# Kernel optimization log

Hardware: AMD Instinct MI355X
Metric: run time of the kernel (lower is better)

Reference implementation:

```python
import jax, jax.numpy as jnp
import numpy as np


def _mlp(x, Ws):
    # torch Linear(bias=False): y = x @ W.T, then leaky_relu (slope 0.01)
    for W in Ws:
        x = jax.nn.leaky_relu(x @ W.T)
    return x


def setup_inputs() -> dict:
    key = jax.random.key(0)
    ks = jax.random.split(key, 17)
    B, Cm, Hm = 128, 512, 28
    D = 2048  # NET_OUT_DIM['resnet50']
    shapes = {
        'x_mid': (B, Cm, Hm, Hm),
        'x_deep': (B, D, 7, 7),
        'w_shallow': (D, Cm),
        'ow1': (1024, D), 'ow2': (512, 1024), 'ow3': (64, 512),
        'sw1': (1024, D), 'sw2': (512, 1024), 'sw3': (64, 512),
        'tw1': (64, 128), 'tw2': (64, 64),
        'cw1': (64, 128), 'cw2': (64, 64),
        'qw1': (64, 64), 'qw2': (64, 64),
        'center': (64,), 'proto': (4, 64),
    }
    out = {}
    for k, (name, shp) in zip(ks, shapes.items()):
        scale = 1.0 if name in ('x_mid', 'x_deep', 'center', 'proto') else 0.02
        out[name] = jax.random.normal(k, shp, dtype=jnp.float32) * scale
    return out


def reference(x_mid, x_deep, w_shallow, ow1, ow2, ow3, sw1, sw2, sw3,
              tw1, tw2, cw1, cw2, qw1, qw2, center, proto):
    # shallow_conv: 1x1 conv Cm -> D
    shallow_map = jnp.einsum('bchw,oc->bohw', x_mid, w_shallow)
    # adaptive avgpool (1,1) + flatten == mean over HW
    origin = _mlp(x_deep.mean(axis=(2, 3)), [ow1, ow2, ow3])        # [B,64]
    shallow = _mlp(shallow_map.mean(axis=(2, 3)), [sw1, sw2, sw3])  # [B,64]
    texture = _mlp(jnp.concatenate([shallow, shallow - center[None]], axis=1),
                   [tw1, tw2])                                      # [B,64]
    # squared distances to each domain prototype -> [B, domain_cnt]
    sim = jnp.sum((texture[:, None, :] - proto[None, :, :]) ** 2, axis=-1)
    category = jnp.argmax(sim, axis=1)  # argmax(softmax(x)) == argmax(x)
    logp = jax.nn.log_softmax(sim, axis=1)
    ce = -jnp.mean(jnp.take_along_axis(logp, category[:, None], axis=1))
    # vectorized gather of per-sample prototype (replaces python loop)
    class_feat = jnp.concatenate([origin, origin - proto[category]], axis=1)
    class_feat = _mlp(class_feat, [cw1, cw2])
    class_svdd = jnp.sum((class_feat - center[None]) ** 2, axis=1)
    origin_svdd = jnp.sum((_mlp(origin, [qw1, qw2]) - center[None]) ** 2, axis=1)
    align = jnp.abs(origin_svdd - class_svdd)
    return jnp.stack([ce, origin_svdd.mean(), class_svdd.mean(),
                      align.mean()]).reshape(4, 1)
```

## Files before the change

kernel.cpp:

```cpp
#include <hip/hip_runtime.h>
#include <hip/hip_bf16.h>
#include <math.h>

typedef __attribute__((ext_vector_type(8))) short bf16x8;
typedef __attribute__((ext_vector_type(4))) float f32x4;
typedef __attribute__((ext_vector_type(4))) unsigned short u16x4;

__device__ __forceinline__ float leaky(float x) { return x > 0.0f ? x : 0.01f * x; }

__device__ __forceinline__ unsigned short f2b(float f) {
    unsigned u = __builtin_bit_cast(unsigned, f);
    u += 0x7fffu + ((u >> 16) & 1u);
    return (unsigned short)(u >> 16);
}

__device__ __forceinline__ bf16x8 cvt8(float4 u0, float4 u1) {
    bf16x8 r;
    r[0] = (short)f2b(u0.x); r[1] = (short)f2b(u0.y);
    r[2] = (short)f2b(u0.z); r[3] = (short)f2b(u0.w);
    r[4] = (short)f2b(u1.x); r[5] = (short)f2b(u1.y);
    r[6] = (short)f2b(u1.z); r[7] = (short)f2b(u1.w);
    return r;
}

__global__ __launch_bounds__(256) void prep_kernel(
    const float* __restrict__ xm, const float* __restrict__ xd,
    const float* __restrict__ sw1, const float* __restrict__ wsh,
    unsigned short* __restrict__ Ws1,
    unsigned short* __restrict__ xm_b, unsigned short* __restrict__ xd_b,
    float4* __restrict__ zbase)
{
    const int blk = blockIdx.x;
    const int tid = threadIdx.x;

    if (blk < 256) {
        const int l = tid & 63, lr = l & 15, lc = l >> 4, w = tid >> 6;
        const int m0 = (blk >> 4) * 64 + w * 16;
        const int n0 = (blk & 15) * 32;
        const float* ap = sw1 + (size_t)(m0 + lr) * 2048 + lc * 8;
        f32x4 acc0 = {0.f,0.f,0.f,0.f}, acc1 = {0.f,0.f,0.f,0.f};
        for (int kt = 0; kt < 2048; kt += 32) {
            bf16x8 a = cvt8(*(const float4*)(ap + kt), *(const float4*)(ap + kt + 4));
            bf16x8 b0, b1;
            #pragma unroll
            for (int j = 0; j < 8; ++j) {
                int kk = kt + lc * 8 + j;
                b0[j] = (short)f2b(wsh[(size_t)kk * 512 + n0 + lr]);
                b1[j] = (short)f2b(wsh[(size_t)kk * 512 + n0 + 16 + lr]);
            }
            acc0 = __builtin_amdgcn_mfma_f32_16x16x32_bf16(a, b0, acc0, 0, 0, 0);
            acc1 = __builtin_amdgcn_mfma_f32_16x16x32_bf16(a, b1, acc1, 0, 0, 0);
        }
        #pragma unroll
        for (int r = 0; r < 4; ++r) {
            int m = m0 + lc * 4 + r;
            Ws1[(size_t)m * 512 + n0 + lr]      = f2b(acc0[r]);
            Ws1[(size_t)m * 512 + n0 + 16 + lr] = f2b(acc1[r]);
        }
        return;
    }
    if (blk < 16640) {
        int b2 = blk - 256;
        int lane = tid & 63, wid = tid >> 6;
        int row  = b2 * 4 + wid;
        const float4* r = (const float4*)(xm + (size_t)row * 784);
        float s = 0.0f;
        for (int i = lane; i < 196; i += 64) {
            float4 v = r[i];
            s += v.x + v.y + v.z + v.w;
        }
        #pragma unroll
        for (int off = 32; off; off >>= 1) s += __shfl_xor(s, off);
        if (lane == 0) xm_b[row] = f2b(s * (1.0f / 784.0f));
        return;
    }
    if (blk < 33024) {
        int b3 = blk - 16640;
        int sub = tid & 15, rr = tid >> 4;
        int row = b3 * 16 + rr;
        const float* base = xd + (size_t)row * 49;
        float s = base[sub] + base[sub + 16] + base[sub + 32];
        if (sub == 0) s += base[48];
        #pragma unroll
        for (int off = 8; off; off >>= 1) s += __shfl_xor(s, off);
        if (sub == 0) xd_b[row] = f2b(s * (1.0f / 49.0f));
        return;
    }
    {
        int idx = (blk - 33024) * 256 + tid;
        zbase[idx] = make_float4(0.f, 0.f, 0.f, 0.f);
    }
}

__device__ __forceinline__ void gemm_phase(
    const void* __restrict__ A, int af, int aact,
    const void* __restrict__ B, int bfB,
    float* __restrict__ C,
    int N, int K, int Kc, int k0, int n0,
    unsigned short (*Bs)[72], int tid)
{
    const int l  = tid & 63;
    const int lr = l & 15;
    const int lc = l >> 4;
    const int m0 = (tid >> 6) * 16;
    const int srow = tid >> 4;
    const int scol = (tid & 15) * 4;

    f32x4 acc0 = {0.f,0.f,0.f,0.f}, acc1 = {0.f,0.f,0.f,0.f};

    for (int kt = 0; kt < Kc; kt += 64) {
        if (!bfB) {
            float4 v = *(const float4*)((const float*)B + (size_t)(n0 + srow) * K + k0 + kt + scol);
            __syncthreads();
            Bs[srow][scol + 0] = f2b(v.x);
            Bs[srow][scol + 1] = f2b(v.y);
            Bs[srow][scol + 2] = f2b(v.z);
            Bs[srow][scol + 3] = f2b(v.w);
        } else {
            u16x4 v = *(const u16x4*)((const unsigned short*)B + (size_t)(n0 + srow) * K + k0 + kt + scol);
            __syncthreads();
            Bs[srow][scol + 0] = v.x;
            Bs[srow][scol + 1] = v.y;
            Bs[srow][scol + 2] = v.z;
            Bs[srow][scol + 3] = v.w;
        }
        __syncthreads();

        #pragma unroll
        for (int kc = 0; kc < 2; ++kc) {
            size_t aoff = (size_t)(m0 + lr) * K + k0 + kt + kc * 32 + lc * 8;
            bf16x8 a;
            if (!af) {
                a = *(const bf16x8*)((const unsigned short*)A + aoff);
            } else {
                const float* p = (const float*)A + aoff;
                float4 u0 = *(const float4*)p;
                float4 u1 = *(const float4*)(p + 4);
                if (aact) {
                    u0.x = leaky(u0.x); u0.y = leaky(u0.y);
                    u0.z = leaky(u0.z); u0.w = leaky(u0.w);
                    u1.x = leaky(u1.x); u1.y = leaky(u1.y);
                    u1.z = leaky(u1.z); u1.w = leaky(u1.w);
                }
                a = cvt8(u0, u1);
            }
            bf16x8 b0 = *(const bf16x8*)&Bs[lr][kc * 32 + lc * 8];
            bf16x8 b1 = *(const bf16x8*)&Bs[16 + lr][kc * 32 + lc * 8];
            acc0 = __builtin_amdgcn_mfma_f32_16x16x32_bf16(a, b0, acc0, 0, 0, 0);
            acc1 = __builtin_amdgcn_mfma_f32_16x16x32_bf16(a, b1, acc1, 0, 0, 0);
        }
    }

    #pragma unroll
    for (int r = 0; r < 4; ++r) {
        int m = m0 + lc * 4 + r;
        atomicAdd(&C[(size_t)m * N + n0 + lr],      acc0[r]);
        atomicAdd(&C[(size_t)m * N + n0 + 16 + lr], acc1[r]);
    }
}

__global__ __launch_bounds__(512) void l1_kernel(
    const unsigned short* __restrict__ xd_b, const unsigned short* __restrict__ xm_b,
    const float* __restrict__ ow1, const unsigned short* __restrict__ Ws1,
    float* __restrict__ C2o, float* __restrict__ C2s)
{
    __shared__ unsigned short Bs[32][72];
    const int bid = blockIdx.x, tid = threadIdx.x;
    if (bid < 256) {
        int nt = bid >> 3, s = bid & 7;
        gemm_phase(xd_b, 0, 0, ow1, 0, C2o, 1024, 2048, 256, s * 256, nt * 32, Bs, tid);
    } else {
        int idx = bid - 256, nt = idx >> 2, s = idx & 3;
        gemm_phase(xm_b, 0, 0, Ws1, 1, C2s, 1024, 512, 128, s * 128, nt * 32, Bs, tid);
    }
}

__global__ __launch_bounds__(512) void l2_kernel(
    const float* __restrict__ C2o, const float* __restrict__ C2s,
    const float* __restrict__ ow2, const float* __restrict__ sw2,
    float* __restrict__ C3o, float* __restrict__ C3s)
{
    __shared__ unsigned short Bs[32][72];
    const int bid = blockIdx.x, tid = threadIdx.x;
    const int z = bid >> 7, idx = bid & 127;
    const int nt = idx >> 3, s = idx & 7;
    gemm_phase(z ? (const void*)C2s : (const void*)C2o, 1, 1,
               z ? (const void*)sw2 : (const void*)ow2, 0,
               z ? C3s : C3o, 512, 1024, 128, s * 128, nt * 32, Bs, tid);
}

__global__ __launch_bounds__(256) void tail_kernel(
    const float* __restrict__ C3o, const float* __restrict__ C3s,
    const float* __restrict__ ow3, const float* __restrict__ sw3,
    const float* __restrict__ tw1, const float* __restrict__ tw2,
    const float* __restrict__ cw1, const float* __restrict__ cw2,
    const float* __restrict__ qw1, const float* __restrict__ qw2,
    const float* __restrict__ center, const float* __restrict__ proto,
    int* __restrict__ cnt, float* __restrict__ ce_t, float* __restrict__ osv,
    float* __restrict__ csv, float* __restrict__ alv,
    float* __restrict__ out)
{
    const int b = blockIdx.x;
    const int tid = threadIdx.x;
    __shared__ float o2r[512], s2r[512];
    __shared__ float red[2][64][4];
    __shared__ float o3s[64], s3s[64], t1s[64], c1s[64], q1s[64];
    __shared__ float tmp[4][4];
    __shared__ int flag;

    for (int e = tid; e < 512; e += 256) {
        o2r[e] = leaky(C3o[b * 512 + e]);
        s2r[e] = leaky(C3s[b * 512 + e]);
    }
    __syncthreads();
    {
        int o = (tid >> 2) & 63, q = tid & 3, p = tid >> 8;
        (void)p;
        const float* wro = ow3 + (size_t)o * 512 + q * 128;
        const float* wrs = sw3 + (size_t)o * 512 + q * 128;
        const float* xo = o2r + q * 128;
        const float* xs = s2r + q * 128;
        float ao = 0.f, as_ = 0.f;
        for (int j = 0; j < 128; ++j) {
            ao  += wro[j] * xo[j];
            as_ += wrs[j] * xs[j];
        }
        red[0][o][q] = ao;
        red[1][o][q] = as_;
    }
    __syncthreads();
    if (tid < 128) {
        int p = tid >> 6, o = tid & 63;
        float v = leaky(red[p][o][0] + red[p][o][1] + red[p][o][2] + red[p][o][3]);
        if (p) s3s[o] = v; else o3s[o] = v;
    }
    __syncthreads();

    float ce_val = 0.f;
    int o = tid;
    if (tid < 64) {
        float acc = 0.f;
        for (int j = 0; j < 64; ++j) acc += tw1[o * 128 + j] * s3s[j];
        for (int j = 0; j < 64; ++j) acc += tw1[o * 128 + 64 + j] * (s3s[j] - center[j]);
        t1s[o] = leaky(acc);
    }
    __syncthreads();
    if (tid < 64) {
        float acc = 0.f;
        for (int j = 0; j < 64; ++j) acc += tw2[o * 64 + j] * t1s[j];
        float tex = leaky(acc);
        float sim[4];
        #pragma unroll
        for (int k = 0; k < 4; ++k) {
            float d = tex - proto[k * 64 + o];
            float v = d * d;
            #pragma unroll
            for (int off = 32; off; off >>= 1) v += __shfl_xor(v, off);
            sim[k] = v;
        }
        int cat = 0; float best = sim[0];
        #pragma unroll
        for (int k = 1; k < 4; ++k) if (sim[k] > best) { best = sim[k]; cat = k; }
        float sume = 0.f;
        #pragma unroll
        for (int k = 0; k < 4; ++k) sume += expf(sim[k] - best);
        ce_val = logf(sume);
        float acc2 = 0.f;
        for (int j = 0; j < 64; ++j) acc2 += cw1[o * 128 + j] * o3s[j];
        for (int j = 0; j < 64; ++j) acc2 += cw1[o * 128 + 64 + j] * (o3s[j] - proto[cat * 64 + j]);
        c1s[o] = leaky(acc2);
        acc2 = 0.f;
        for (int j = 0; j < 64; ++j) acc2 += qw1[o * 64 + j] * o3s[j];
        q1s[o] = leaky(acc2);
    }
    __syncthreads();
    if (tid < 64) {
        float acc = 0.f;
        for (int j = 0; j < 64; ++j) acc += cw2[o * 64 + j] * c1s[j];
        float cf = leaky(acc);
        float dc = cf - center[o];
        float cs = dc * dc;
        #pragma unroll
        for (int off = 32; off; off >>= 1) cs += __shfl_xor(cs, off);
        acc = 0.f;
        for (int j = 0; j < 64; ++j) acc += qw2[o * 64 + j] * q1s[j];
        float qf = leaky(acc);
        float dq = qf - center[o];
        float os = dq * dq;
        #pragma unroll
        for (int off = 32; off; off >>= 1) os += __shfl_xor(os, off);
        if (o == 0) {
            __hip_atomic_store(&ce_t[b], ce_val, __ATOMIC_RELAXED, __HIP_MEMORY_SCOPE_AGENT);
            __hip_atomic_store(&osv[b],  os,     __ATOMIC_RELAXED, __HIP_MEMORY_SCOPE_AGENT);
            __hip_atomic_store(&csv[b],  cs,     __ATOMIC_RELAXED, __HIP_MEMORY_SCOPE_AGENT);
            __hip_atomic_store(&alv[b],  fabsf(os - cs), __ATOMIC_RELAXED, __HIP_MEMORY_SCOPE_AGENT);
        }
    }
    __syncthreads();
    if (tid == 0) {
        asm volatile("s_waitcnt vmcnt(0)" ::: "memory");
        int old = __hip_atomic_fetch_add(cnt, 1, __ATOMIC_ACQ_REL, __HIP_MEMORY_SCOPE_AGENT);
        flag = (old == 127);
    }
    __syncthreads();
    if (flag) {
        float v0 = 0.f, v1 = 0.f, v2 = 0.f, v3 = 0.f;
        if (tid < 128) {
            v0 = __hip_atomic_load(&ce_t[tid], __ATOMIC_RELAXED, __HIP_MEMORY_SCOPE_AGENT);
            v1 = __hip_atomic_load(&osv[tid],  __ATOMIC_RELAXED, __HIP_MEMORY_SCOPE_AGENT);
            v2 = __hip_atomic_load(&csv[tid],  __ATOMIC_RELAXED, __HIP_MEMORY_SCOPE_AGENT);
            v3 = __hip_atomic_load(&alv[tid],  __ATOMIC_RELAXED, __HIP_MEMORY_SCOPE_AGENT);
        }
        float v[4] = { v0, v1, v2, v3 };
        int lane = tid & 63, wv = tid >> 6;
        #pragma unroll
        for (int i = 0; i < 4; ++i) {
            float x = v[i];
            #pragma unroll
            for (int off = 32; off; off >>= 1) x += __shfl_xor(x, off);
            if (lane == 0) tmp[i][wv] = x;
        }
        __syncthreads();
        if (tid < 4) {
            float s = 0.f;
            #pragma unroll
            for (int j = 0; j < 4; ++j) s += tmp[tid][j];
            out[tid] = s * (1.0f / 128.0f);
        }
    }
}

extern "C" void kernel_launch(void* const* d_in, const int* in_sizes, int n_in,
                              void* d_out, int out_size, void* d_ws, size_t ws_size,
                              hipStream_t stream)
{
    const float* x_mid     = (const float*)d_in[0];
    const float* x_deep    = (const float*)d_in[1];
    const float* w_shallow = (const float*)d_in[2];
    const float* ow1 = (const float*)d_in[3];
    const float* ow2 = (const float*)d_in[4];
    const float* ow3 = (const float*)d_in[5];
    const float* sw1 = (const float*)d_in[6];
    const float* sw2 = (const float*)d_in[7];
    const float* sw3 = (const float*)d_in[8];
    const float* tw1 = (const float*)d_in[9];
    const float* tw2 = (const float*)d_in[10];
    const float* cw1 = (const float*)d_in[11];
    const float* cw2 = (const float*)d_in[12];
    const float* qw1 = (const float*)d_in[13];
    const float* qw2 = (const float*)d_in[14];
    const float* center = (const float*)d_in[15];
    const float* proto  = (const float*)d_in[16];
    float* out = (float*)d_out;

    float* wf = (float*)d_ws;
    float* C2o = wf;
    float* C2s = wf + 131072;
    float* C3o = wf + 262144;
    float* C3s = wf + 327680;
    int*   cnt = (int*)(wf + 393216);
    float* ce_t = wf + 393472;
    float* osv  = ce_t + 128;
    float* csv  = ce_t + 256;
    float* alv  = ce_t + 384;
    unsigned short* Ws1  = (unsigned short*)(wf + 394240);
    unsigned short* xm_b = Ws1 + 524288;
    unsigned short* xd_b = xm_b + 65536;

    prep_kernel<<<33409, 256, 0, stream>>>(x_mid, x_deep, sw1, w_shallow,
                                           Ws1, xm_b, xd_b, (float4*)wf);

    l1_kernel<<<384, 512, 0, stream>>>(xd_b, xm_b, ow1, Ws1, C2o, C2s);

    l2_kernel<<<256, 512, 0, stream>>>(C2o, C2s, ow2, sw2, C3o, C3s);

    tail_kernel<<<128, 256, 0, stream>>>(C3o, C3s, ow3, sw3, tw1, tw2, cw1, cw2,
                                         qw1, qw2, center, proto,
                                         cnt, ce_t, osv, csv, alv, out);
}
```

Before: 99.94 us.

## Fuse GEMM layers and tail into one kernel with flag-gated stages

Merges the two GEMM layer kernels and the tail kernel into a single 768-block launch. Later stages spin on global counter and flag words before reading earlier results, which removes two kernel launch boundaries. The prep kernel's weight-fold GEMM is also retiled into 32 larger blocks, each computing a 128x128 tile so A and B fragments are reused more. The spin-wait relies on all producer blocks being resident or scheduled first, which carries a deadlock or stall risk, and the retiled fold runs on far fewer blocks.

New measurement: 169.3 us. 1.69x slower.

```diff
diff --git a/kernel.cpp b/kernel.cpp
--- a/kernel.cpp
+++ b/kernel.cpp
@@ -33,34 +33,55 @@
     const int blk = blockIdx.x;
     const int tid = threadIdx.x;
 
-    if (blk < 256) {
+    if (blk < 32) {
+        const int mb = blk >> 2, nb = blk & 3;
         const int l = tid & 63, lr = l & 15, lc = l >> 4, w = tid >> 6;
-        const int m0 = (blk >> 4) * 64 + w * 16;
-        const int n0 = (blk & 15) * 32;
-        const float* ap = sw1 + (size_t)(m0 + lr) * 2048 + lc * 8;
-        f32x4 acc0 = {0.f,0.f,0.f,0.f}, acc1 = {0.f,0.f,0.f,0.f};
+        const int m0 = mb * 128 + w * 32;
+        const int n0 = nb * 128;
+        const float* ap0 = sw1 + (size_t)(m0 + lr) * 2048 + lc * 8;
+        const float* ap1 = ap0 + (size_t)16 * 2048;
+        f32x4 acc[2][4][2];
+        #pragma unroll
+        for (int a = 0; a < 2; ++a)
+            #pragma unroll
+            for (int b = 0; b < 4; ++b)
+                #pragma unroll
+                for (int c = 0; c < 2; ++c) acc[a][b][c] = (f32x4){0.f,0.f,0.f,0.f};
+
         for (int kt = 0; kt < 2048; kt += 32) {
-            bf16x8 a = cvt8(*(const float4*)(ap + kt), *(const float4*)(ap + kt + 4));
-            bf16x8 b0, b1;
-            #pragma unroll
-            for (int j = 0; j < 8; ++j) {
-                int kk = kt + lc * 8 + j;
-                b0[j] = (short)f2b(wsh[(size_t)kk * 512 + n0 + lr]);
-                b1[j] = (short)f2b(wsh[(size_t)kk * 512 + n0 + 16 + lr]);
+            bf16x8 a0 = cvt8(*(const float4*)(ap0 + kt), *(const float4*)(ap0 + kt + 4));
+            bf16x8 a1 = cvt8(*(const float4*)(ap1 + kt), *(const float4*)(ap1 + kt + 4));
+            #pragma unroll
+            for (int nf = 0; nf < 4; ++nf) {
+                bf16x8 b0, b1;
+                #pragma unroll
+                for (int j = 0; j < 8; ++j) {
+                    const float* bp = wsh + (size_t)(kt + lc * 8 + j) * 512 + n0 + nf * 32 + lr;
+                    b0[j] = (short)f2b(bp[0]);
+                    b1[j] = (short)f2b(bp[16]);
+                }
+                acc[0][nf][0] = __builtin_amdgcn_mfma_f32_16x16x32_bf16(a0, b0, acc[0][nf][0], 0, 0, 0);
+                acc[0][nf][1] = __builtin_amdgcn_mfma_f32_16x16x32_bf16(a0, b1, acc[0][nf][1], 0, 0, 0);
+                acc[1][nf][0] = __builtin_amdgcn_mfma_f32_16x16x32_bf16(a1, b0, acc[1][nf][0], 0, 0, 0);
+                acc[1][nf][1] = __builtin_amdgcn_mfma_f32_16x16x32_bf16(a1, b1, acc[1][nf][1], 0, 0, 0);
             }
-            acc0 = __builtin_amdgcn_mfma_f32_16x16x32_bf16(a, b0, acc0, 0, 0, 0);
-            acc1 = __builtin_amdgcn_mfma_f32_16x16x32_bf16(a, b1, acc1, 0, 0, 0);
-        }
-        #pragma unroll
-        for (int r = 0; r < 4; ++r) {
-            int m = m0 + lc * 4 + r;
-            Ws1[(size_t)m * 512 + n0 + lr]      = f2b(acc0[r]);
-            Ws1[(size_t)m * 512 + n0 + 16 + lr] = f2b(acc1[r]);
-        }
-        return;
-    }
-    if (blk < 16640) {
-        int b2 = blk - 256;
+        }
+        #pragma unroll
+        for (int mf = 0; mf < 2; ++mf)
+            #pragma unroll
+            for (int nf = 0; nf < 4; ++nf)
+                #pragma unroll
+                for (int p = 0; p < 2; ++p)
+                    #pragma unroll
+                    for (int r = 0; r < 4; ++r) {
+                        int m = m0 + mf * 16 + lc * 4 + r;
+                        int n = n0 + nf * 32 + p * 16 + lr;
+                        Ws1[(size_t)m * 512 + n] = f2b(acc[mf][nf][p][r]);
+                    }
+        return;
+    }
+    if (blk < 16416) {
+        int b2 = blk - 32;
         int lane = tid & 63, wid = tid >> 6;
         int row  = b2 * 4 + wid;
         const float4* r = (const float4*)(xm + (size_t)row * 784);
@@ -74,8 +95,8 @@
         if (lane == 0) xm_b[row] = f2b(s * (1.0f / 784.0f));
         return;
     }
-    if (blk < 33024) {
-        int b3 = blk - 16640;
+    if (blk < 32800) {
+        int b3 = blk - 16416;
         int sub = tid & 15, rr = tid >> 4;
         int row = b3 * 16 + rr;
         const float* base = xd + (size_t)row * 49;
@@ -87,8 +108,27 @@
         return;
     }
     {
-        int idx = (blk - 33024) * 256 + tid;
+        int idx = (blk - 32800) * 256 + tid;
         zbase[idx] = make_float4(0.f, 0.f, 0.f, 0.f);
+    }
+}
+
+__device__ __forceinline__ void gate(const int* flag) {
+    if (threadIdx.x == 0) {
+        while (__hip_atomic_load(flag, __ATOMIC_RELAXED, __HIP_MEMORY_SCOPE_AGENT) == 0)
+            __builtin_amdgcn_s_sleep(32);
+    }
+    __syncthreads();
+    __builtin_amdgcn_fence(__ATOMIC_ACQUIRE, "agent");
+}
+
+__device__ __forceinline__ void done(int* cnt, int target, int* flag) {
+    __syncthreads();
+    if (threadIdx.x == 0) {
+        asm volatile("s_waitcnt vmcnt(0)" ::: "memory");
+        int old = __hip_atomic_fetch_add(cnt, 1, __ATOMIC_RELAXED, __HIP_MEMORY_SCOPE_AGENT);
+        if (old == target - 1)
+            __hip_atomic_store(flag, 1, __ATOMIC_RELAXED, __HIP_MEMORY_SCOPE_AGENT);
     }
 }
 
@@ -159,74 +199,81 @@
     }
 }
 
-__global__ __launch_bounds__(512) void l1_kernel(
-    const unsigned short* __restrict__ xd_b, const unsigned short* __restrict__ xm_b,
-    const float* __restrict__ ow1, const unsigned short* __restrict__ Ws1,
-    float* __restrict__ C2o, float* __restrict__ C2s)
-{
-    __shared__ unsigned short Bs[32][72];
-    const int bid = blockIdx.x, tid = threadIdx.x;
-    if (bid < 256) {
-        int nt = bid >> 3, s = bid & 7;
-        gemm_phase(xd_b, 0, 0, ow1, 0, C2o, 1024, 2048, 256, s * 256, nt * 32, Bs, tid);
-    } else {
-        int idx = bid - 256, nt = idx >> 2, s = idx & 3;
-        gemm_phase(xm_b, 0, 0, Ws1, 1, C2s, 1024, 512, 128, s * 128, nt * 32, Bs, tid);
-    }
-}
-
-__global__ __launch_bounds__(512) void l2_kernel(
-    const float* __restrict__ C2o, const float* __restrict__ C2s,
-    const float* __restrict__ ow2, const float* __restrict__ sw2,
-    float* __restrict__ C3o, float* __restrict__ C3s)
-{
-    __shared__ unsigned short Bs[32][72];
-    const int bid = blockIdx.x, tid = threadIdx.x;
-    const int z = bid >> 7, idx = bid & 127;
-    const int nt = idx >> 3, s = idx & 7;
-    gemm_phase(z ? (const void*)C2s : (const void*)C2o, 1, 1,
-               z ? (const void*)sw2 : (const void*)ow2, 0,
-               z ? C3s : C3o, 512, 1024, 128, s * 128, nt * 32, Bs, tid);
-}
-
-__global__ __launch_bounds__(256) void tail_kernel(
-    const float* __restrict__ C3o, const float* __restrict__ C3s,
-    const float* __restrict__ ow3, const float* __restrict__ sw3,
+__global__ __launch_bounds__(512, 4) void fused_kernel(
+    float* __restrict__ wf,
+    const unsigned short* __restrict__ xm_b, const unsigned short* __restrict__ xd_b,
+    const unsigned short* __restrict__ Ws1,
+    const float* __restrict__ ow1, const float* __restrict__ ow2, const float* __restrict__ ow3,
+    const float* __restrict__ sw2, const float* __restrict__ sw3,
     const float* __restrict__ tw1, const float* __restrict__ tw2,
     const float* __restrict__ cw1, const float* __restrict__ cw2,
     const float* __restrict__ qw1, const float* __restrict__ qw2,
     const float* __restrict__ center, const float* __restrict__ proto,
-    int* __restrict__ cnt, float* __restrict__ ce_t, float* __restrict__ osv,
-    float* __restrict__ csv, float* __restrict__ alv,
     float* __restrict__ out)
 {
-    const int b = blockIdx.x;
-    const int tid = threadIdx.x;
+    __shared__ unsigned short Bs[32][72];
     __shared__ float o2r[512], s2r[512];
     __shared__ float red[2][64][4];
     __shared__ float o3s[64], s3s[64], t1s[64], c1s[64], q1s[64];
-    __shared__ float tmp[4][4];
-    __shared__ int flag;
-
-    for (int e = tid; e < 512; e += 256) {
+    __shared__ float tmp[4][8];
+    __shared__ int flag_sh;
+
+    float* C2o = wf;
+    float* C2s = wf + 131072;
+    float* C3o = wf + 262144;
+    float* C3s = wf + 327680;
+    int*   cntL1  = (int*)(wf + 393216);
+    int*   flagL1 = (int*)(wf + 393216 + 32);
+    int*   cntL2  = (int*)(wf + 393216 + 64);
+    int*   flagL2 = (int*)(wf + 393216 + 96);
+    int*   cntT   = (int*)(wf + 393216 + 128);
+    float* ce_t = wf + 393472;
+    float* osv  = ce_t + 128;
+    float* csv  = ce_t + 256;
+    float* alv  = ce_t + 384;
+
+    const int bid = blockIdx.x;
+    const int tid = threadIdx.x;
+
+    if (bid < 256) {
+        int nt = bid >> 3, s = bid & 7;
+        gemm_phase(xd_b, 0, 0, ow1, 0, C2o, 1024, 2048, 256, s * 256, nt * 32, Bs, tid);
+        done(cntL1, 384, flagL1);
+        return;
+    }
+    if (bid < 384) {
+        int idx = bid - 256, nt = idx >> 2, s = idx & 3;
+        gemm_phase(xm_b, 0, 0, Ws1, 1, C2s, 1024, 512, 128, s * 128, nt * 32, Bs, tid);
+        done(cntL1, 384, flagL1);
+        return;
+    }
+    if (bid < 640) {
+        gate(flagL1);
+        int b3 = bid - 384;
+        int z = b3 >> 7, idx = b3 & 127, nt = idx >> 3, s = idx & 7;
+        gemm_phase(z ? (const void*)C2s : (const void*)C2o, 1, 1,
+                   z ? (const void*)sw2 : (const void*)ow2, 0,
+                   z ? C3s : C3o, 512, 1024, 128, s * 128, nt * 32, Bs, tid);
+        done(cntL2, 256, flagL2);
+        return;
+    }
+
+    const int b = bid - 640;
+    gate(flagL2);
+
+    {
+        int e = tid;
         o2r[e] = leaky(C3o[b * 512 + e]);
         s2r[e] = leaky(C3s[b * 512 + e]);
     }
     __syncthreads();
     {
-        int o = (tid >> 2) & 63, q = tid & 3, p = tid >> 8;
-        (void)p;
-        const float* wro = ow3 + (size_t)o * 512 + q * 128;
-        const float* wrs = sw3 + (size_t)o * 512 + q * 128;
-        const float* xo = o2r + q * 128;
-        const float* xs = s2r + q * 128;
-        float ao = 0.f, as_ = 0.f;
-        for (int j = 0; j < 128; ++j) {
-            ao  += wro[j] * xo[j];
-            as_ += wrs[j] * xs[j];
-        }
-        red[0][o][q] = ao;
-        red[1][o][q] = as_;
+        int p = tid >> 8, o = (tid >> 2) & 63, q = tid & 3;
+        const float* wr = (p ? sw3 : ow3) + (size_t)o * 512 + q * 128;
+        const float* xr = (p ? s2r : o2r) + q * 128;
+        float acc = 0.f;
+        for (int j = 0; j < 128; ++j) acc += wr[j] * xr[j];
+        red[p][o][q] = acc;
     }
     __syncthreads();
     if (tid < 128) {
@@ -299,11 +346,11 @@
     __syncthreads();
     if (tid == 0) {
         asm volatile("s_waitcnt vmcnt(0)" ::: "memory");
-        int old = __hip_atomic_fetch_add(cnt, 1, __ATOMIC_ACQ_REL, __HIP_MEMORY_SCOPE_AGENT);
-        flag = (old == 127);
-    }
-    __syncthreads();
-    if (flag) {
+        int old = __hip_atomic_fetch_add(cntT, 1, __ATOMIC_ACQ_REL, __HIP_MEMORY_SCOPE_AGENT);
+        flag_sh = (old == 127);
+    }
+    __syncthreads();
+    if (flag_sh) {
         float v0 = 0.f, v1 = 0.f, v2 = 0.f, v3 = 0.f;
         if (tid < 128) {
             v0 = __hip_atomic_load(&ce_t[tid], __ATOMIC_RELAXED, __HIP_MEMORY_SCOPE_AGENT);
@@ -324,7 +371,7 @@
         if (tid < 4) {
             float s = 0.f;
             #pragma unroll
-            for (int j = 0; j < 4; ++j) s += tmp[tid][j];
+            for (int j = 0; j < 8; ++j) s += tmp[tid][j];
             out[tid] = s * (1.0f / 128.0f);
         }
     }
@@ -354,27 +401,15 @@
     float* out = (float*)d_out;
 
     float* wf = (float*)d_ws;
-    float* C2o = wf;
-    float* C2s = wf + 131072;
-    float* C3o = wf + 262144;
-    float* C3s = wf + 327680;
-    int*   cnt = (int*)(wf + 393216);
-    float* ce_t = wf + 393472;
-    float* osv  = ce_t + 128;
-    float* csv  = ce_t + 256;
-    float* alv  = ce_t + 384;
     unsigned short* Ws1  = (unsigned short*)(wf + 394240);
     unsigned short* xm_b = Ws1 + 524288;
     unsigned short* xd_b = xm_b + 65536;
 
-    prep_kernel<<<33409, 256, 0, stream>>>(x_mid, x_deep, sw1, w_shallow,
+    prep_kernel<<<33185, 256, 0, stream>>>(x_mid, x_deep, sw1, w_shallow,
                                            Ws1, xm_b, xd_b, (float4*)wf);
 
-    l1_kernel<<<384, 512, 0, stream>>>(xd_b, xm_b, ow1, Ws1, C2o, C2s);
-
-    l2_kernel<<<256, 512, 0, stream>>>(C2o, C2s, ow2, sw2, C3o, C3s);
-
-    tail_kernel<<<128, 256, 0, stream>>>(C3o, C3s, ow3, sw3, tw1, tw2, cw1, cw2,
-                                         qw1, qw2, center, proto,
-                                         cnt, ce_t, osv, csv, alv, out);
-}
+    fused_kernel<<<768, 512, 0, stream>>>(wf, xm_b, xd_b, Ws1,
+                                          ow1, ow2, ow3, sw2, sw3,
+                                          tw1, tw2, cw1, cw2, qw1, qw2,
+                                          center, proto, out);
+}
```
